# Performance work log

Measured on AMD Instinct MI355X. Metric: run time of the kernel, lower is better.

The kernel has to match this reference:

```python
import jax, jax.numpy as jnp
import numpy as np

N_NODES = 50000
N_EDGES = 800000
IN_DIM = 128
HID_DIM = 256
N_CLASS = 40
PROP_STEP = 3
DROPOUT = 0.0  # eval-mode drop_node scale = (1 - DROPOUT)


def setup_inputs() -> dict:
    key = jax.random.key(0)
    k = jax.random.split(key, 6)
    features = jax.random.normal(k[0], (N_NODES, IN_DIM), dtype=jnp.float32)
    src = jax.random.randint(k[1], (N_EDGES,), 0, N_NODES)
    dst = jax.random.randint(k[2], (N_EDGES,), 0, N_NODES)
    W1 = jax.random.normal(k[3], (IN_DIM, HID_DIM), dtype=jnp.float32) / np.sqrt(IN_DIM)
    b1 = jnp.zeros((HID_DIM,), dtype=jnp.float32)
    W2 = jax.random.normal(k[4], (HID_DIM, N_CLASS), dtype=jnp.float32) / np.sqrt(HID_DIM)
    b2 = jnp.zeros((N_CLASS,), dtype=jnp.float32)
    return {"features": features, "src": src, "dst": dst,
            "W1": W1, "b1": b1, "W2": W2, "b2": b2}


def reference(features, src, dst, W1, b1, W2, b2):
    N = features.shape[0]
    # in-degree-based symmetric normalization: norm = deg^{-1/2}, deg clamped to >= 1
    degs = jax.ops.segment_sum(jnp.ones_like(dst, dtype=jnp.float32), dst,
                               num_segments=N)
    norm = jnp.clip(degs, 1.0, None) ** -0.5              # [N]
    w = norm[src] * norm[dst]                             # [E] edge weights (u_mul_v)

    # eval-mode drop_node: scale features by (1 - drop_rate)
    x = features * (1.0 - DROPOUT)
    y = x
    for _ in range(PROP_STEP):
        # u_mul_e: gather source features, scale by edge weight, scatter-sum to dst
        m = x[src] * w[:, None]                           # [E, F]
        x = jax.ops.segment_sum(m, dst, num_segments=N)   # [N, F]
        y = y + x
    feat = y / (PROP_STEP + 1)

    # MLP (use_bn=False, dropouts are 0 / eval): relu(linear) -> linear
    h = jax.nn.relu(feat @ W1 + b1)
    logits = h @ W2 + b2
    return jax.nn.log_softmax(logits, axis=-1)
```

## Files before the change

kernel.cpp:

```cpp
#include <hip/hip_runtime.h>

#define IN_DIM 128
#define HID    256
#define NCLS   40
#define BSHIFT 8
#define BSZ    256
#define MAXNB  256
#define CHUNK  4096

static inline size_t align256(size_t x) { return (x + 255) & ~(size_t)255; }

typedef __attribute__((ext_vector_type(2))) float f32x2;

__device__ inline unsigned pack_bf16x2(float x, float y) {
    unsigned xb = __float_as_uint(x), yb = __float_as_uint(y);
    unsigned lo = (xb + 0x7fffu + ((xb >> 16) & 1u)) >> 16;
    unsigned hi = (yb + 0x7fffu + ((yb >> 16) & 1u)) >> 16;
    return lo | (hi << 16);
}
__device__ inline unsigned short f2bf(float x) {
    unsigned b = __float_as_uint(x);
    return (unsigned short)((b + 0x7fffu + ((b >> 16) & 1u)) >> 16);
}

__device__ inline unsigned pack_fp8x4(float a, float b, float c, float d) {
    int v = __builtin_amdgcn_cvt_pk_fp8_f32(a, b, 0, false);
    v = __builtin_amdgcn_cvt_pk_fp8_f32(c, d, v, true);
    return (unsigned)v;
}

__global__ __launch_bounds__(256) void bucket_count_kernel(
        const int* __restrict__ dst, int* __restrict__ bucketCnt, int E, int NB) {
    __shared__ int hist[MAXNB];
    int t = threadIdx.x;
    hist[t] = 0;
    __syncthreads();
    int start = blockIdx.x * CHUNK;
    int cnt = min(CHUNK, E - start);
    for (int i = t; i < cnt; i += 256) atomicAdd(&hist[dst[start + i] >> BSHIFT], 1);
    __syncthreads();
    if (t < NB && hist[t]) atomicAdd(&bucketCnt[t], hist[t]);
}

__global__ __launch_bounds__(256) void bucket_scan_kernel(
        const int* __restrict__ bucketCnt, int* __restrict__ bucketBase,
        int* __restrict__ bucketCursor, int* __restrict__ offs, int NB, int N) {
    int t = threadIdx.x, lane = t & 63, wave = t >> 6;
    int v = (t < NB) ? bucketCnt[t] : 0;
    int s = v;
    for (int off = 1; off < 64; off <<= 1) {
        int u = __shfl_up(s, off, 64);
        if (lane >= off) s += u;
    }
    __shared__ int wsum[4];
    if (lane == 63) wsum[wave] = s;
    __syncthreads();
    if (t == 0) {
        int c = 0;
        for (int i = 0; i < 4; ++i) { int x = wsum[i]; wsum[i] = c; c += x; }
    }
    __syncthreads();
    int incl = wsum[wave] + s;
    int excl = incl - v;
    if (t < NB) { bucketBase[t] = excl; bucketCursor[t] = excl; }
    if (t == NB - 1) { bucketBase[NB] = incl; offs[N] = incl; }
}

__global__ __launch_bounds__(256) void bucket_scatter_kernel(
        const int* __restrict__ src, const int* __restrict__ dst,
        int* __restrict__ bucketCursor, int2* __restrict__ ebuf, int E) {
    __shared__ int hist[MAXNB], lofs[MAXNB], lcur[MAXNB], gbase[MAXNB];
    __shared__ int2 bin[CHUNK];
    int t = threadIdx.x, lane = t & 63, wave = t >> 6;
    int start = blockIdx.x * CHUNK;
    int cnt = min(CHUNK, E - start);
    hist[t] = 0;
    __syncthreads();
    for (int i = t; i < cnt; i += 256) atomicAdd(&hist[dst[start + i] >> BSHIFT], 1);
    __syncthreads();
    int v = hist[t];
    int s = v;
    for (int off = 1; off < 64; off <<= 1) {
        int u = __shfl_up(s, off, 64);
        if (lane >= off) s += u;
    }
    __shared__ int wsum[4];
    if (lane == 63) wsum[wave] = s;
    __syncthreads();
    if (t == 0) {
        int c = 0;
        for (int i = 0; i < 4; ++i) { int x = wsum[i]; wsum[i] = c; c += x; }
    }
    __syncthreads();
    int excl = wsum[wave] + s - v;
    lofs[t] = excl; lcur[t] = excl;
    if (v) gbase[t] = atomicAdd(&bucketCursor[t], v);
    __syncthreads();
    for (int i = t; i < cnt; i += 256) {
        int s0 = src[start + i], d0 = dst[start + i];
        int r = atomicAdd(&lcur[d0 >> BSHIFT], 1);
        bin[r] = make_int2(s0, d0);
    }
    __syncthreads();
    for (int i = t; i < cnt; i += 256) {
        int2 e = bin[i];
        int b = e.y >> BSHIFT;
        ebuf[gbase[b] + i - lofs[b]] = e;
    }
}

__global__ __launch_bounds__(256) void build_norm_kernel(
        const int2* __restrict__ ebuf, const int* __restrict__ bucketBase,
        int* __restrict__ offs, float* __restrict__ norm, int N) {
    __shared__ int hist[BSZ];
    int b = blockIdx.x, t = threadIdx.x, lane = t & 63, wave = t >> 6;
    hist[t] = 0;
    __syncthreads();
    int segS = bucketBase[b], segE = bucketBase[b + 1];
    for (int i = segS + t; i < segE; i += 256) atomicAdd(&hist[ebuf[i].y & (BSZ - 1)], 1);
    __syncthreads();
    int v = hist[t];
    int s = v;
    for (int off = 1; off < 64; off <<= 1) {
        int u = __shfl_up(s, off, 64);
        if (lane >= off) s += u;
    }
    __shared__ int wsum[4];
    if (lane == 63) wsum[wave] = s;
    __syncthreads();
    if (t == 0) {
        int c = 0;
        for (int i = 0; i < 4; ++i) { int x = wsum[i]; wsum[i] = c; c += x; }
    }
    __syncthreads();
    int excl = wsum[wave] + s - v;
    int node = b * BSZ + t;
    if (node < N) {
        offs[node] = segS + excl;
        norm[node] = rsqrtf((float)(v > 0 ? v : 1));
    }
}

__global__ __launch_bounds__(256) void build_csr_kernel(
        const int2* __restrict__ ebuf, const int* __restrict__ bucketBase,
        const int* __restrict__ offs, const float* __restrict__ norm,
        int2* __restrict__ csr, int N) {
    __shared__ int lcur[BSZ];
    __shared__ float snorm[BSZ];
    int b = blockIdx.x, t = threadIdx.x;
    int node = b * BSZ + t;
    lcur[t] = (node < N) ? offs[node] : 0;
    snorm[t] = (node < N) ? norm[node] : 0.f;
    __syncthreads();
    int segS = bucketBase[b], segE = bucketBase[b + 1];
    for (int i = segS + t; i < segE; i += 256) {
        int2 e = ebuf[i];
        int li = e.y & (BSZ - 1);
        float w = norm[e.x] * snorm[li];
        int p = atomicAdd(&lcur[li], 1);
        csr[p] = make_int2(e.x, __float_as_int(w));
    }
}

__global__ void prep_kernel(const float* __restrict__ feat, unsigned* __restrict__ x0,
                            const float* __restrict__ W1, const float* __restrict__ W2,
                            unsigned short* __restrict__ W1T, unsigned short* __restrict__ W2T,
                            int nfeat_dw) {
    int i = blockIdx.x * blockDim.x + threadIdx.x;
    if (i < nfeat_dw) {
        float4 f = *(const float4*)(feat + (size_t)i * 4);
        x0[i] = pack_fp8x4(f.x, f.y, f.z, f.w);
        return;
    }
    int j = i - nfeat_dw;
    if (j < 256 * 128) {
        int n = j >> 7, k = j & 127;
        W1T[j] = f2bf(W1[k * 256 + n]);
        return;
    }
    int k2 = j - 256 * 128;
    if (k2 < 48 * 256) {
        int c = k2 >> 8, kk = k2 & 255;
        W2T[k2] = (c < 40) ? f2bf(W2[kk * 40 + c]) : (unsigned short)0;
    }
}

#define ACCP(dd, ww)                                                          \
    {                                                                         \
        f32x2 wv2 = {(ww), (ww)};                                             \
        c0 += __builtin_amdgcn_cvt_pk_f32_fp8((int)(dd).x, false) * wv2;      \
        c1 += __builtin_amdgcn_cvt_pk_f32_fp8((int)(dd).x, true ) * wv2;      \
        c2 += __builtin_amdgcn_cvt_pk_f32_fp8((int)(dd).y, false) * wv2;      \
        c3 += __builtin_amdgcn_cvt_pk_f32_fp8((int)(dd).y, true ) * wv2;      \
    }

__global__ __launch_bounds__(256) void prop_kernel(
        const unsigned* __restrict__ xin, unsigned* __restrict__ xout,
        const int* __restrict__ offs, const int2* __restrict__ csr, int N) {
    int t = threadIdx.x;
    int wv = t >> 6, lane = t & 63;
    int q = lane >> 4, ql = lane & 15;
    int v = blockIdx.x * 4 + wv;
    if (v >= N) return;
    __shared__ int2 sIW[4][64];
    int start = offs[v], end = offs[v + 1];
    f32x2 c0 = {0.f, 0.f}, c1 = {0.f, 0.f}, c2 = {0.f, 0.f}, c3 = {0.f, 0.f};
    for (int k = start; k < end; k += 64) {
        int cnt = min(64, end - k);
        if (lane < cnt) sIW[wv][lane] = csr[k + lane];
        int j = 0;
        for (; j + 16 <= cnt; j += 16) {
            uint2 d[4]; float w[4];
#pragma unroll
            for (int u = 0; u < 4; ++u) {
                int2 e = sIW[wv][j + 4 * u + q];
                w[u] = __int_as_float(e.y);
                d[u] = *(const uint2*)(xin + (size_t)e.x * 32 + ql * 2);
            }
#pragma unroll
            for (int u = 0; u < 4; ++u) ACCP(d[u], w[u]);
        }
        int rem = cnt - j;
        if (rem > 8) {
            uint2 d[4]; float w[4];
#pragma unroll
            for (int u = 0; u < 4; ++u) {
                int idx = j + 4 * u + q;
                int2 e = sIW[wv][min(idx, cnt - 1)];
                w[u] = (idx < cnt) ? __int_as_float(e.y) : 0.f;
                d[u] = *(const uint2*)(xin + (size_t)e.x * 32 + ql * 2);
            }
#pragma unroll
            for (int u = 0; u < 4; ++u) ACCP(d[u], w[u]);
        } else if (rem > 0) {
            uint2 d[2]; float w[2];
#pragma unroll
            for (int u = 0; u < 2; ++u) {
                int idx = j + 4 * u + q;
                int2 e = sIW[wv][min(idx, cnt - 1)];
                w[u] = (idx < cnt) ? __int_as_float(e.y) : 0.f;
                d[u] = *(const uint2*)(xin + (size_t)e.x * 32 + ql * 2);
            }
#pragma unroll
            for (int u = 0; u < 2; ++u) ACCP(d[u], w[u]);
        }
    }
    float a0 = c0.x, a1 = c0.y, a2 = c1.x, a3 = c1.y;
    float a4 = c2.x, a5 = c2.y, a6 = c3.x, a7 = c3.y;
    a0 += __shfl_xor(a0, 16, 64); a0 += __shfl_xor(a0, 32, 64);
    a1 += __shfl_xor(a1, 16, 64); a1 += __shfl_xor(a1, 32, 64);
    a2 += __shfl_xor(a2, 16, 64); a2 += __shfl_xor(a2, 32, 64);
    a3 += __shfl_xor(a3, 16, 64); a3 += __shfl_xor(a3, 32, 64);
    a4 += __shfl_xor(a4, 16, 64); a4 += __shfl_xor(a4, 32, 64);
    a5 += __shfl_xor(a5, 16, 64); a5 += __shfl_xor(a5, 32, 64);
    a6 += __shfl_xor(a6, 16, 64); a6 += __shfl_xor(a6, 32, 64);
    a7 += __shfl_xor(a7, 16, 64); a7 += __shfl_xor(a7, 32, 64);
    if (q == 0) {
        uint2 o;
        o.x = pack_fp8x4(a0, a1, a2, a3);
        o.y = pack_fp8x4(a4, a5, a6, a7);
        *(uint2*)(xout + (size_t)v * 32 + ql * 2) = o;
    }
}

typedef __attribute__((ext_vector_type(8))) short bf16x8;
typedef __attribute__((ext_vector_type(4))) float f32x4;

#define SA_STRIDE 136
#define SH_STRIDE 264

__device__ inline void unpack8(uint2 u, float* q) {
    f32x2 p;
    p = __builtin_amdgcn_cvt_pk_f32_fp8((int)u.x, false); q[0] = p.x; q[1] = p.y;
    p = __builtin_amdgcn_cvt_pk_f32_fp8((int)u.x, true ); q[2] = p.x; q[3] = p.y;
    p = __builtin_amdgcn_cvt_pk_f32_fp8((int)u.y, false); q[4] = p.x; q[5] = p.y;
    p = __builtin_amdgcn_cvt_pk_f32_fp8((int)u.y, true ); q[6] = p.x; q[7] = p.y;
}

__global__ __launch_bounds__(256) void mlp16_kernel(
        const float* __restrict__ feat, const unsigned* __restrict__ x1,
        const unsigned* __restrict__ x2, const unsigned* __restrict__ x3,
        const unsigned short* __restrict__ W1T, const float* __restrict__ b1,
        const unsigned short* __restrict__ W2T, const float* __restrict__ b2,
        float* __restrict__ out, int N) {
    __shared__ unsigned short sA[16 * SA_STRIDE];
    __shared__ unsigned short sH[16 * SH_STRIDE];
    int t = threadIdx.x, wv = t >> 6, lane = t & 63;
    int l15 = lane & 15, lq = lane >> 4;
    int base = blockIdx.x * 16;

    {
        int n = t >> 4, sg = t & 15;
        int gv = base + n;
        uint4 o = make_uint4(0u, 0u, 0u, 0u);
        if (gv < N) {
            size_t fo = (size_t)gv * 128 + sg * 8;
            float4 f0 = *(const float4*)(feat + fo);
            float4 f1 = *(const float4*)(feat + fo + 4);
            uint2 u1 = *(const uint2*)(x1 + (size_t)gv * 32 + sg * 2);
            uint2 u2 = *(const uint2*)(x2 + (size_t)gv * 32 + sg * 2);
            uint2 u3 = *(const uint2*)(x3 + (size_t)gv * 32 + sg * 2);
            float q1[8], q2[8], q3[8];
            unpack8(u1, q1); unpack8(u2, q2); unpack8(u3, q3);
            float ff[8] = {f0.x, f0.y, f0.z, f0.w, f1.x, f1.y, f1.z, f1.w};
            float s[8];
#pragma unroll
            for (int i = 0; i < 8; ++i) s[i] = (ff[i] + q1[i] + q2[i] + q3[i]) * 0.25f;
            o.x = pack_bf16x2(s[0], s[1]); o.y = pack_bf16x2(s[2], s[3]);
            o.z = pack_bf16x2(s[4], s[5]); o.w = pack_bf16x2(s[6], s[7]);
        }
        *(uint4*)&sA[n * SA_STRIDE + sg * 8] = o;
    }
    __syncthreads();

    f32x4 acc[4];
#pragma unroll
    for (int ht = 0; ht < 4; ++ht) acc[ht] = (f32x4){0.f, 0.f, 0.f, 0.f};
#pragma unroll
    for (int s = 0; s < 4; ++s) {
        bf16x8 afr = *(const bf16x8*)&sA[l15 * SA_STRIDE + s * 32 + lq * 8];
#pragma unroll
        for (int ht = 0; ht < 4; ++ht) {
            bf16x8 bfr = *(const bf16x8*)(W1T + ((wv * 64 + ht * 16 + l15) * 128 + s * 32 + lq * 8));
            acc[ht] = __builtin_amdgcn_mfma_f32_16x16x32_bf16(afr, bfr, acc[ht], 0, 0, 0);
        }
    }
#pragma unroll
    for (int ht = 0; ht < 4; ++ht) {
        int hid = wv * 64 + ht * 16 + l15;
        float bb = b1[hid];
#pragma unroll
        for (int r = 0; r < 4; ++r) {
            int node = lq * 4 + r;
            sH[node * SH_STRIDE + hid] = f2bf(fmaxf(acc[ht][r] + bb, 0.f));
        }
    }
    __syncthreads();
    if (wv != 0) return;

    f32x4 acc2[3];
#pragma unroll
    for (int ct = 0; ct < 3; ++ct) acc2[ct] = (f32x4){0.f, 0.f, 0.f, 0.f};
#pragma unroll
    for (int s = 0; s < 8; ++s) {
        bf16x8 afr = *(const bf16x8*)&sH[l15 * SH_STRIDE + s * 32 + lq * 8];
#pragma unroll
        for (int ct = 0; ct < 3; ++ct) {
            bf16x8 bfr = *(const bf16x8*)(W2T + ((ct * 16 + l15) * 256 + s * 32 + lq * 8));
            acc2[ct] = __builtin_amdgcn_mfma_f32_16x16x32_bf16(afr, bfr, acc2[ct], 0, 0, 0);
        }
    }

    float lg[3][4];
#pragma unroll
    for (int ct = 0; ct < 3; ++ct) {
        int c = ct * 16 + l15;
        float bb = (c < NCLS) ? b2[c] : 0.f;
#pragma unroll
        for (int r = 0; r < 4; ++r) lg[ct][r] = acc2[ct][r] + bb;
    }
#pragma unroll
    for (int r = 0; r < 4; ++r) {
        float m = fmaxf(lg[0][r], lg[1][r]);
        if (l15 < 8) m = fmaxf(m, lg[2][r]);
        for (int off = 1; off < 16; off <<= 1) m = fmaxf(m, __shfl_xor(m, off, 64));
        float ssum = __expf(lg[0][r] - m) + __expf(lg[1][r] - m) +
                     ((l15 < 8) ? __expf(lg[2][r] - m) : 0.f);
        for (int off = 1; off < 16; off <<= 1) ssum += __shfl_xor(ssum, off, 64);
        float ls = m + __logf(ssum);
        int node = base + lq * 4 + r;
        if (node < N) {
#pragma unroll
            for (int ct = 0; ct < 3; ++ct) {
                int c = ct * 16 + l15;
                if (c < NCLS) out[(size_t)node * NCLS + c] = lg[ct][r] - ls;
            }
        }
    }
}

extern "C" void kernel_launch(void* const* d_in, const int* in_sizes, int n_in,
                              void* d_out, int out_size, void* d_ws, size_t ws_size,
                              hipStream_t stream) {
    const float* feat = (const float*)d_in[0];
    const int*   src  = (const int*)d_in[1];
    const int*   dst  = (const int*)d_in[2];
    const float* W1   = (const float*)d_in[3];
    const float* b1   = (const float*)d_in[4];
    const float* W2   = (const float*)d_in[5];
    const float* b2   = (const float*)d_in[6];
    float* out = (float*)d_out;

    int N = in_sizes[0] / IN_DIM;
    int E = in_sizes[1];
    int NB = (N + BSZ - 1) / BSZ;

    char* ws = (char*)d_ws;
    size_t off = 0;
    float* norm   = (float*)(ws + off); off += align256((size_t)N * 4);
    int*   offs   = (int*)(ws + off);   off += align256((size_t)(N + 1) * 4);
    int*   bBase  = (int*)(ws + off);   off += align256((size_t)(MAXNB + 1) * 4);
    int*   bCur   = (int*)(ws + off);   off += align256((size_t)MAXNB * 4);
    int*   bCnt   = (int*)(ws + off);   off += align256((size_t)MAXNB * 4);
    int2*  csr    = (int2*)(ws + off);  off += align256((size_t)E * 8);
    unsigned* x0  = (unsigned*)(ws + off); off += align256((size_t)N * 32 * 4);
    unsigned* x1  = (unsigned*)(ws + off); off += align256((size_t)N * 32 * 4);
    unsigned* x2  = (unsigned*)(ws + off); off += align256((size_t)N * 32 * 4);
    unsigned* x3  = (unsigned*)(ws + off); off += align256((size_t)N * 32 * 4);
    int2*  ebuf   = (int2*)(ws + off);  off += align256((size_t)E * 8);
    unsigned short* W1T = (unsigned short*)(ws + off); off += align256((size_t)256 * 128 * 2);
    unsigned short* W2T = (unsigned short*)(ws + off); off += align256((size_t)48 * 256 * 2);
    (void)ws_size;

    hipMemsetAsync(bCnt, 0, (size_t)MAXNB * 4, stream);

    int echunks = (E + CHUNK - 1) / CHUNK;
    bucket_count_kernel<<<echunks, 256, 0, stream>>>(dst, bCnt, E, NB);
    bucket_scan_kernel<<<1, 256, 0, stream>>>(bCnt, bBase, bCur, offs, NB, N);
    bucket_scatter_kernel<<<echunks, 256, 0, stream>>>(src, dst, bCur, ebuf, E);
    build_norm_kernel<<<NB, 256, 0, stream>>>(ebuf, bBase, offs, norm, N);
    build_csr_kernel<<<NB, 256, 0, stream>>>(ebuf, bBase, offs, norm, csr, N);

    int nprep = N * 32 + 256 * 128 + 48 * 256;
    prep_kernel<<<(nprep + 255) / 256, 256, 0, stream>>>(feat, x0, W1, W2, W1T, W2T, N * 32);

    int pb = (N + 3) / 4;
    prop_kernel<<<pb, 256, 0, stream>>>(x0, x1, offs, csr, N);
    prop_kernel<<<pb, 256, 0, stream>>>(x1, x2, offs, csr, N);
    prop_kernel<<<pb, 256, 0, stream>>>(x2, x3, offs, csr, N);

    mlp16_kernel<<<(N + 15) / 16, 256, 0, stream>>>(feat, x1, x2, x3,
                                                    W1T, b1, W2T, b2, out, N);
}
```

Before: 224.7 us.

## Process two nodes per wavefront with 16-byte gathers and split MLP layer-2 across waves

The propagation kernel now assigns half a wavefront (32 lanes) to each destination node, with 8 lanes covering a 128-byte fp8 row through uint4 loads and 4 edge groups reduced by shuffles. This halves the grid and widens each gather so more edges are in flight per wave and fewer lanes sit idle on low-degree nodes. Separately, the MLP second layer spreads its three class tiles over three waves, staging logits in shared memory before wave 0 runs the softmax. The cost is more accumulator registers per lane and an extra barrier plus shared-memory round trip in the MLP.

```diff
diff --git a/kernel.cpp b/kernel.cpp
--- a/kernel.cpp
+++ b/kernel.cpp
@@ -185,81 +185,87 @@
     }
 }
 
-#define ACCP(dd, ww)                                                          \
+#define ACCP16(dd, ww)                                                        \
     {                                                                         \
         f32x2 wv2 = {(ww), (ww)};                                             \
         c0 += __builtin_amdgcn_cvt_pk_f32_fp8((int)(dd).x, false) * wv2;      \
         c1 += __builtin_amdgcn_cvt_pk_f32_fp8((int)(dd).x, true ) * wv2;      \
         c2 += __builtin_amdgcn_cvt_pk_f32_fp8((int)(dd).y, false) * wv2;      \
         c3 += __builtin_amdgcn_cvt_pk_f32_fp8((int)(dd).y, true ) * wv2;      \
-    }
+        c4 += __builtin_amdgcn_cvt_pk_f32_fp8((int)(dd).z, false) * wv2;      \
+        c5 += __builtin_amdgcn_cvt_pk_f32_fp8((int)(dd).z, true ) * wv2;      \
+        c6 += __builtin_amdgcn_cvt_pk_f32_fp8((int)(dd).w, false) * wv2;      \
+        c7 += __builtin_amdgcn_cvt_pk_f32_fp8((int)(dd).w, true ) * wv2;      \
+    }
+
+#define RED2(a) { a += __shfl_xor(a, 8, 64); a += __shfl_xor(a, 16, 64); }
 
 __global__ __launch_bounds__(256) void prop_kernel(
         const unsigned* __restrict__ xin, unsigned* __restrict__ xout,
         const int* __restrict__ offs, const int2* __restrict__ csr, int N) {
     int t = threadIdx.x;
     int wv = t >> 6, lane = t & 63;
-    int q = lane >> 4, ql = lane & 15;
-    int v = blockIdx.x * 4 + wv;
+    int h = lane >> 5, hl = lane & 31;
+    int g = hl >> 3, gl = hl & 7;
+    int v = blockIdx.x * 8 + wv * 2 + h;
     if (v >= N) return;
-    __shared__ int2 sIW[4][64];
+    __shared__ int2 sIW[4][2][32];
     int start = offs[v], end = offs[v + 1];
-    f32x2 c0 = {0.f, 0.f}, c1 = {0.f, 0.f}, c2 = {0.f, 0.f}, c3 = {0.f, 0.f};
-    for (int k = start; k < end; k += 64) {
-        int cnt = min(64, end - k);
-        if (lane < cnt) sIW[wv][lane] = csr[k + lane];
+    f32x2 c0 = {0.f,0.f}, c1 = {0.f,0.f}, c2 = {0.f,0.f}, c3 = {0.f,0.f};
+    f32x2 c4 = {0.f,0.f}, c5 = {0.f,0.f}, c6 = {0.f,0.f}, c7 = {0.f,0.f};
+    for (int k = start; k < end; k += 32) {
+        int cnt = min(32, end - k);
+        if (hl < cnt) sIW[wv][h][hl] = csr[k + hl];
         int j = 0;
         for (; j + 16 <= cnt; j += 16) {
-            uint2 d[4]; float w[4];
+            uint4 d[4]; float w[4];
 #pragma unroll
             for (int u = 0; u < 4; ++u) {
-                int2 e = sIW[wv][j + 4 * u + q];
+                int2 e = sIW[wv][h][j + 4 * u + g];
                 w[u] = __int_as_float(e.y);
-                d[u] = *(const uint2*)(xin + (size_t)e.x * 32 + ql * 2);
+                d[u] = *(const uint4*)(xin + (size_t)e.x * 32 + gl * 4);
             }
 #pragma unroll
-            for (int u = 0; u < 4; ++u) ACCP(d[u], w[u]);
+            for (int u = 0; u < 4; ++u) ACCP16(d[u], w[u]);
         }
         int rem = cnt - j;
         if (rem > 8) {
-            uint2 d[4]; float w[4];
+            uint4 d[4]; float w[4];
 #pragma unroll
             for (int u = 0; u < 4; ++u) {
-                int idx = j + 4 * u + q;
-                int2 e = sIW[wv][min(idx, cnt - 1)];
+                int idx = j + 4 * u + g;
+                int2 e = sIW[wv][h][min(idx, cnt - 1)];
                 w[u] = (idx < cnt) ? __int_as_float(e.y) : 0.f;
-                d[u] = *(const uint2*)(xin + (size_t)e.x * 32 + ql * 2);
+                d[u] = *(const uint4*)(xin + (size_t)e.x * 32 + gl * 4);
             }
 #pragma unroll
-            for (int u = 0; u < 4; ++u) ACCP(d[u], w[u]);
+            for (int u = 0; u < 4; ++u) ACCP16(d[u], w[u]);
         } else if (rem > 0) {
-            uint2 d[2]; float w[2];
+            uint4 d[2]; float w[2];
 #pragma unroll
             for (int u = 0; u < 2; ++u) {
-                int idx = j + 4 * u + q;
-                int2 e = sIW[wv][min(idx, cnt - 1)];
+                int idx = j + 4 * u + g;
+                int2 e = sIW[wv][h][min(idx, cnt - 1)];
                 w[u] = (idx < cnt) ? __int_as_float(e.y) : 0.f;
-                d[u] = *(const uint2*)(xin + (size_t)e.x * 32 + ql * 2);
+                d[u] = *(const uint4*)(xin + (size_t)e.x * 32 + gl * 4);
             }
 #pragma unroll
-            for (int u = 0; u < 2; ++u) ACCP(d[u], w[u]);
+            for (int u = 0; u < 2; ++u) ACCP16(d[u], w[u]);
         }
     }
     float a0 = c0.x, a1 = c0.y, a2 = c1.x, a3 = c1.y;
     float a4 = c2.x, a5 = c2.y, a6 = c3.x, a7 = c3.y;
-    a0 += __shfl_xor(a0, 16, 64); a0 += __shfl_xor(a0, 32, 64);
-    a1 += __shfl_xor(a1, 16, 64); a1 += __shfl_xor(a1, 32, 64);
-    a2 += __shfl_xor(a2, 16, 64); a2 += __shfl_xor(a2, 32, 64);
-    a3 += __shfl_xor(a3, 16, 64); a3 += __shfl_xor(a3, 32, 64);
-    a4 += __shfl_xor(a4, 16, 64); a4 += __shfl_xor(a4, 32, 64);
-    a5 += __shfl_xor(a5, 16, 64); a5 += __shfl_xor(a5, 32, 64);
-    a6 += __shfl_xor(a6, 16, 64); a6 += __shfl_xor(a6, 32, 64);
-    a7 += __shfl_xor(a7, 16, 64); a7 += __shfl_xor(a7, 32, 64);
-    if (q == 0) {
-        uint2 o;
+    float a8 = c4.x, a9 = c4.y, a10 = c5.x, a11 = c5.y;
+    float a12 = c6.x, a13 = c6.y, a14 = c7.x, a15 = c7.y;
+    RED2(a0); RED2(a1); RED2(a2); RED2(a3); RED2(a4); RED2(a5); RED2(a6); RED2(a7);
+    RED2(a8); RED2(a9); RED2(a10); RED2(a11); RED2(a12); RED2(a13); RED2(a14); RED2(a15);
+    if (g == 0) {
+        uint4 o;
         o.x = pack_fp8x4(a0, a1, a2, a3);
         o.y = pack_fp8x4(a4, a5, a6, a7);
-        *(uint2*)(xout + (size_t)v * 32 + ql * 2) = o;
+        o.z = pack_fp8x4(a8, a9, a10, a11);
+        o.w = pack_fp8x4(a12, a13, a14, a15);
+        *(uint4*)(xout + (size_t)v * 32 + gl * 4) = o;
     }
 }
 
@@ -285,6 +291,7 @@
         float* __restrict__ out, int N) {
     __shared__ unsigned short sA[16 * SA_STRIDE];
     __shared__ unsigned short sH[16 * SH_STRIDE];
+    __shared__ float sLog[16][49];
     int t = threadIdx.x, wv = t >> 6, lane = t & 63;
     int l15 = lane & 15, lq = lane >> 4;
     int base = blockIdx.x * 16;
@@ -336,29 +343,29 @@
         }
     }
     __syncthreads();
-    if (wv != 0) return;
-
-    f32x4 acc2[3];
-#pragma unroll
-    for (int ct = 0; ct < 3; ++ct) acc2[ct] = (f32x4){0.f, 0.f, 0.f, 0.f};
-#pragma unroll
-    for (int s = 0; s < 8; ++s) {
-        bf16x8 afr = *(const bf16x8*)&sH[l15 * SH_STRIDE + s * 32 + lq * 8];
-#pragma unroll
-        for (int ct = 0; ct < 3; ++ct) {
+
+    if (wv < 3) {
+        int ct = wv;
+        f32x4 acc2 = (f32x4){0.f, 0.f, 0.f, 0.f};
+#pragma unroll
+        for (int s = 0; s < 8; ++s) {
+            bf16x8 afr = *(const bf16x8*)&sH[l15 * SH_STRIDE + s * 32 + lq * 8];
             bf16x8 bfr = *(const bf16x8*)(W2T + ((ct * 16 + l15) * 256 + s * 32 + lq * 8));
-            acc2[ct] = __builtin_amdgcn_mfma_f32_16x16x32_bf16(afr, bfr, acc2[ct], 0, 0, 0);
-        }
-    }
-
-    float lg[3][4];
-#pragma unroll
-    for (int ct = 0; ct < 3; ++ct) {
+            acc2 = __builtin_amdgcn_mfma_f32_16x16x32_bf16(afr, bfr, acc2, 0, 0, 0);
+        }
         int c = ct * 16 + l15;
         float bb = (c < NCLS) ? b2[c] : 0.f;
 #pragma unroll
-        for (int r = 0; r < 4; ++r) lg[ct][r] = acc2[ct][r] + bb;
-    }
+        for (int r = 0; r < 4; ++r) sLog[lq * 4 + r][c] = acc2[r] + bb;
+    }
+    __syncthreads();
+    if (wv != 0) return;
+
+    float lg[3][4];
+#pragma unroll
+    for (int ct = 0; ct < 3; ++ct)
+#pragma unroll
+        for (int r = 0; r < 4; ++r) lg[ct][r] = sLog[lq * 4 + r][ct * 16 + l15];
 #pragma unroll
     for (int r = 0; r < 4; ++r) {
         float m = fmaxf(lg[0][r], lg[1][r]);
@@ -424,7 +431,7 @@
     int nprep = N * 32 + 256 * 128 + 48 * 256;
     prep_kernel<<<(nprep + 255) / 256, 256, 0, stream>>>(feat, x0, W1, W2, W1T, W2T, N * 32);
 
-    int pb = (N + 3) / 4;
+    int pb = (N + 7) / 8;
     prop_kernel<<<pb, 256, 0, stream>>>(x0, x1, offs, csr, N);
     prop_kernel<<<pb, 256, 0, stream>>>(x1, x2, offs, csr, N);
     prop_kernel<<<pb, 256, 0, stream>>>(x2, x3, offs, csr, N);
```

New measurement: 218.0 us. 1.03x faster.
